# Kernel optimization log

Hardware: AMD Instinct MI355X
Metric: run time of the kernel (lower is better)

## Reference

```python
import jax, jax.numpy as jnp
import numpy as np

VOCAB, EMB, HID = 50257, 256, 512
B, S = 64, 512


def setup_inputs() -> dict:
    key = jax.random.key(0)
    ks = jax.random.split(key, 11)
    sc = 0.05
    return {
        "inputs": jax.random.randint(ks[0], (B, S), 0, VOCAB, dtype=jnp.int32),
        "emb": jax.random.normal(ks[1], (VOCAB, EMB), jnp.float32) * sc,
        "Wi": jax.random.normal(ks[2], (EMB, 4 * HID), jnp.float32) * sc,   # kernel, gate order i|f|g|o (Keras)
        "Wh": jax.random.normal(ks[3], (HID, 4 * HID), jnp.float32) * sc,   # recurrent kernel
        "b": jax.random.normal(ks[4], (4 * HID,), jnp.float32) * sc,
        "W1": jax.random.normal(ks[5], (HID, HID), jnp.float32) * sc,
        "b1": jnp.zeros((HID,), jnp.float32),
        "W2": jax.random.normal(ks[6], (HID, HID), jnp.float32) * sc,
        "b2": jnp.zeros((HID,), jnp.float32),
        "W3": jax.random.normal(ks[7], (HID, VOCAB), jnp.float32) * sc,
        "b3": jnp.zeros((VOCAB,), jnp.float32),
    }


def _lstm_final_h(x, Wi, Wh, b):
    # x: [B, S, E] -> final hidden state [B, H]
    Bsz = x.shape[0]
    H = Wh.shape[0]
    h0 = jnp.zeros((Bsz, H), x.dtype)
    c0 = jnp.zeros((Bsz, H), x.dtype)

    def step(carry, xt):
        h, c = carry
        z = xt @ Wi + h @ Wh + b              # [B, 4H]
        i, f, g, o = jnp.split(z, 4, axis=-1)  # Keras gate order: input, forget, cell, output
        i = jax.nn.sigmoid(i)
        f = jax.nn.sigmoid(f)
        g = jnp.tanh(g)
        o = jax.nn.sigmoid(o)
        c = f * c + i * g
        h = o * jnp.tanh(c)
        return (h, c), None

    (h, _), _ = jax.lax.scan(step, (h0, c0), jnp.swapaxes(x, 0, 1))  # scan over time [S, B, E]
    return h


def reference(inputs, emb, Wi, Wh, b, W1, b1, W2, b2, W3, b3):
    src_emb = emb[inputs]                      # [B, S, E] embedding lookup
    enc_hidden = _lstm_final_h(src_emb, Wi, Wh, b)  # [B, H]
    y = jnp.tanh(enc_hidden @ W1 + b1)
    y = jnp.tanh(y @ W2 + b2)
    logits = y @ W3 + b3                       # [B, vocab]
    return jax.nn.log_softmax(logits, axis=-1)
```

## Files before the change

### kernel.cpp

```cpp
#include <hip/hip_runtime.h>
#include <hip/hip_bf16.h>

#define VOCAB 50257
#define EMBD  256
#define HID   512
#define BATCH 64
#define SEQ   512

typedef short bf16x8 __attribute__((ext_vector_type(8)));
typedef float f32x4  __attribute__((ext_vector_type(4)));

__device__ inline short f2b(float f) {
    union { float f; unsigned u; } v; v.f = f;
    unsigned r = v.u + 0x7FFFu + ((v.u >> 16) & 1u);
    return (short)(r >> 16);
}
__device__ inline unsigned pack2_trunc(float lo, float hi) {
    union { float f; unsigned u; } a, b; a.f = lo; b.f = hi;
    return __builtin_amdgcn_perm(b.u, a.u, 0x07060302);
}
__device__ inline float fast_tanh(float x) {
    x = fminf(fmaxf(x, -15.f), 15.f);
    float e = __expf(2.f * x);
    return (e - 1.f) / (e + 1.f);
}
__device__ inline float fast_sig(float x) { return 1.f / (1.f + __expf(-x)); }

__device__ inline void load_x_frags(const float* __restrict__ emb, int idxv, int quad, bf16x8* Ax) {
#pragma unroll
    for (int kt = 0; kt < 8; ++kt) {
        const float* p = emb + (size_t)idxv * EMBD + kt * 32 + quad * 8;
        float4 e0 = *(const float4*)(p);
        float4 e1 = *(const float4*)(p + 4);
        union { bf16x8 v; unsigned u[4]; } f;
        f.u[0] = pack2_trunc(e0.x, e0.y);
        f.u[1] = pack2_trunc(e0.z, e0.w);
        f.u[2] = pack2_trunc(e1.x, e1.y);
        f.u[3] = pack2_trunc(e1.z, e1.w);
        Ax[kt] = f.v;
    }
}

__global__ __launch_bounds__(256, 1) void lstm_kernel(
    const int* __restrict__ idx, const float* __restrict__ emb,
    const float* __restrict__ Wi, const float* __restrict__ Wh,
    const float* __restrict__ bvec,
    unsigned long long* __restrict__ hbuf ,
    unsigned short* __restrict__ hfinal )
{
    const int wgid = blockIdx.x;
    const int grp  = wgid >> 5;
    const int j    = wgid & 31;
    const int tid  = threadIdx.x;
    const int lane = tid & 63;
    const int gate = tid >> 6;
    const int quad = lane >> 4;
    const int l16  = lane & 15;
    const int col  = gate * HID + j * 16 + l16;
    const int arow = grp * 16 + l16;

    __shared__ float gbuf[4][16][16];
    __shared__ __align__(16) unsigned short hstage[16][HID + 8];

    bf16x8 Bh[16], Bx[8];
#pragma unroll
    for (int kt = 0; kt < 16; ++kt)
#pragma unroll
        for (int i = 0; i < 8; ++i)
            Bh[kt][i] = f2b(Wh[(size_t)(kt * 32 + quad * 8 + i) * 2048 + col]);
#pragma unroll
    for (int kt = 0; kt < 8; ++kt)
#pragma unroll
        for (int i = 0; i < 8; ++i)
            Bx[kt][i] = f2b(Wi[(size_t)(kt * 32 + quad * 8 + i) * 2048 + col]);
    const float bv = bvec[col];

    bf16x8 Ax[8];
    load_x_frags(emb, idx[arow * SEQ], quad, Ax);

    const int srow = gate * 4 + quad;

    const int rr = tid >> 3, u8 = tid & 7, c2 = u8 * 2;
    float cs0 = 0.f, cs1 = 0.f;

    for (int t = 0; t < SEQ; ++t) {
        const unsigned long long* rbase =
            hbuf + ((size_t)((t & 1) * 4 + grp) * 16 + srow) * 256 + l16;

        unsigned long long v[16];
        if (t > 0) {
#pragma unroll
            for (int i = 0; i < 16; ++i)
                v[i] = __hip_atomic_load(rbase + i * 16,
                                         __ATOMIC_RELAXED, __HIP_MEMORY_SCOPE_AGENT);
        }

        f32x4 a0 = {0.f, 0.f, 0.f, 0.f}, a1 = {0.f, 0.f, 0.f, 0.f};
#pragma unroll
        for (int kt = 0; kt < 8; kt += 2) {
            a0 = __builtin_amdgcn_mfma_f32_16x16x32_bf16(Ax[kt],     Bx[kt],     a0, 0, 0, 0);
            a1 = __builtin_amdgcn_mfma_f32_16x16x32_bf16(Ax[kt + 1], Bx[kt + 1], a1, 0, 0, 0);
        }

        if (t > 0) {
            const unsigned tg = (unsigned)t;
            while (true) {
                bool ok = true;
#pragma unroll
                for (int i = 0; i < 16; ++i)
                    ok = ok && ((unsigned)(v[i] >> 32) == tg);
                if (__ballot(ok) == ~0ull) break;
#pragma unroll
                for (int i = 0; i < 16; ++i)
                    v[i] = __hip_atomic_load(rbase + i * 16,
                                             __ATOMIC_RELAXED, __HIP_MEMORY_SCOPE_AGENT);
            }
#pragma unroll
            for (int i = 0; i < 16; ++i)
                *(unsigned*)&hstage[srow][(l16 + i * 16) * 2] = (unsigned)v[i];
        }
        __syncthreads();

        if (t > 0) {
#pragma unroll
            for (int kt = 0; kt < 16; kt += 2) {
                bf16x8 ha = *(const bf16x8*)&hstage[l16][kt * 32 + quad * 8];
                bf16x8 hb = *(const bf16x8*)&hstage[l16][(kt + 1) * 32 + quad * 8];
                a0 = __builtin_amdgcn_mfma_f32_16x16x32_bf16(ha, Bh[kt],     a0, 0, 0, 0);
                a1 = __builtin_amdgcn_mfma_f32_16x16x32_bf16(hb, Bh[kt + 1], a1, 0, 0, 0);
            }
        }

#pragma unroll
        for (int r = 0; r < 4; ++r) {
            float z = a0[r] + a1[r] + bv;
            gbuf[gate][quad * 4 + r][l16] = (gate == 2) ? fast_tanh(z) : fast_sig(z);
        }
        __syncthreads();

        if (tid < 128) {
            float h0, h1;
            {
                float i0 = gbuf[0][rr][c2], f0 = gbuf[1][rr][c2];
                float gg = gbuf[2][rr][c2], o0 = gbuf[3][rr][c2];
                float cc = f0 * cs0 + i0 * gg;
                cs0 = cc;
                h0 = o0 * fast_tanh(cc);
            }
            {
                float i1 = gbuf[0][rr][c2 + 1], f1 = gbuf[1][rr][c2 + 1];
                float gg = gbuf[2][rr][c2 + 1], o1 = gbuf[3][rr][c2 + 1];
                float cc = f1 * cs1 + i1 * gg;
                cs1 = cc;
                h1 = o1 * fast_tanh(cc);
            }
            unsigned pv = (unsigned)(unsigned short)f2b(h0) |
                          ((unsigned)(unsigned short)f2b(h1) << 16);
            unsigned long long val = (unsigned long long)pv |
                                     ((unsigned long long)(unsigned)(t + 1) << 32);
            unsigned long long* dst = hbuf +
                ((size_t)(((t + 1) & 1) * 4 + grp) * 16 + rr) * 256 + j * 8 + u8;
            __hip_atomic_store(dst, val, __ATOMIC_RELAXED, __HIP_MEMORY_SCOPE_AGENT);
            if (t == SEQ - 1)
                *(unsigned*)&hfinal[(size_t)(grp * 16 + rr) * HID + j * 16 + c2] = pv;
        }

        if (t + 1 < SEQ) {
            int nx = idx[arow * SEQ + t + 1];
            load_x_frags(emb, nx, quad, Ax);
        }
    }
}

__global__ __launch_bounds__(256, 1) void gemm_tanh_kernel(
    const unsigned short* __restrict__ A, const float* __restrict__ W,
    const float* __restrict__ bias, unsigned short* __restrict__ out)
{
    const int tid = threadIdx.x, lane = tid & 63, wave = tid >> 6;
    const int quad = lane >> 4, l16 = lane & 15;
    const int col = blockIdx.x * 16 + l16;
    bf16x8 Bw[16];
#pragma unroll
    for (int kt = 0; kt < 16; ++kt)
#pragma unroll
        for (int i = 0; i < 8; ++i)
            Bw[kt][i] = f2b(W[(size_t)(kt * 32 + quad * 8 + i) * HID + col]);
    f32x4 acc = {0.f, 0.f, 0.f, 0.f};
#pragma unroll
    for (int kt = 0; kt < 16; ++kt) {
        bf16x8 a = *(const bf16x8*)(A + (size_t)(wave * 16 + l16) * HID + kt * 32 + quad * 8);
        acc = __builtin_amdgcn_mfma_f32_16x16x32_bf16(a, Bw[kt], acc, 0, 0, 0);
    }
    const float bvv = bias[col];
#pragma unroll
    for (int r = 0; r < 4; ++r) {
        float y = fast_tanh(acc[r] + bvv);
        out[(size_t)(wave * 16 + quad * 4 + r) * HID + col] = (unsigned short)f2b(y);
    }
}

__global__ __launch_bounds__(256, 2) void logits_kernel(
    const unsigned short* __restrict__ A, const float* __restrict__ W3,
    const float* __restrict__ b3, float* __restrict__ outL)
{
    const int tid = threadIdx.x, lane = tid & 63, wave = tid >> 6;
    const int quad = lane >> 4, l16 = lane & 15;
    const int c0 = blockIdx.x * 64;
    const int col = c0 + wave * 16 + l16;
    const bool cok = col < VOCAB;
    const int colc = cok ? col : (VOCAB - 1);

    __shared__ unsigned short wt[256][68];

    f32x4 acc[4];
#pragma unroll
    for (int rt = 0; rt < 4; ++rt) acc[rt] = (f32x4){0.f, 0.f, 0.f, 0.f};

    const int kr = tid >> 4;
    const int cg = (tid & 15) * 4;

    for (int kc = 0; kc < 2; ++kc) {
#pragma unroll 4
        for (int it = 0; it < 16; ++it) {
            const int k = it * 16 + kr;
            const int gc = c0 + cg;
            float4 wv;
            if (gc + 3 < VOCAB) {
                wv = *(const float4*)&W3[(size_t)(kc * 256 + k) * VOCAB + gc];
            } else {
                const float* Wr = &W3[(size_t)(kc * 256 + k) * VOCAB];
                wv.x = (gc + 0 < VOCAB) ? Wr[gc + 0] : 0.f;
                wv.y = (gc + 1 < VOCAB) ? Wr[gc + 1] : 0.f;
                wv.z = (gc + 2 < VOCAB) ? Wr[gc + 2] : 0.f;
                wv.w = (gc + 3 < VOCAB) ? Wr[gc + 3] : 0.f;
            }
            unsigned short* d = &wt[k][cg];
            d[0] = (unsigned short)f2b(wv.x);
            d[1] = (unsigned short)f2b(wv.y);
            d[2] = (unsigned short)f2b(wv.z);
            d[3] = (unsigned short)f2b(wv.w);
        }
        __syncthreads();
        bf16x8 Bw[8];
#pragma unroll
        for (int kt = 0; kt < 8; ++kt)
#pragma unroll
            for (int i = 0; i < 8; ++i)
                Bw[kt][i] = (short)wt[kt * 32 + quad * 8 + i][wave * 16 + l16];
#pragma unroll
        for (int rt = 0; rt < 4; ++rt)
#pragma unroll
            for (int kt = 0; kt < 8; ++kt) {
                bf16x8 a = *(const bf16x8*)(A + (size_t)(rt * 16 + l16) * HID +
                                            kc * 256 + kt * 32 + quad * 8);
                acc[rt] = __builtin_amdgcn_mfma_f32_16x16x32_bf16(a, Bw[kt], acc[rt], 0, 0, 0);
            }
        __syncthreads();
    }
    const float bvv = b3[colc];
    if (cok) {
#pragma unroll
        for (int rt = 0; rt < 4; ++rt)
#pragma unroll
            for (int r = 0; r < 4; ++r)
                outL[(size_t)(rt * 16 + quad * 4 + r) * VOCAB + col] = acc[rt][r] + bvv;
    }
}

__global__ __launch_bounds__(256, 1) void lsm_kernel(
    const float* __restrict__ lg, float* __restrict__ out)
{
    const int row = blockIdx.x;
    const float* L = lg + (size_t)row * VOCAB;
    const float4* L4 = (const float4*)L;
    const int nv4 = VOCAB / 4;

    float m = -1e30f;
    for (int i = threadIdx.x; i < nv4; i += 256) {
        float4 v = L4[i];
        m = fmaxf(fmaxf(fmaxf(m, v.x), fmaxf(v.y, v.z)), v.w);
    }
    if (threadIdx.x == 0) m = fmaxf(m, L[VOCAB - 1]);
#pragma unroll
    for (int o = 32; o; o >>= 1) m = fmaxf(m, __shfl_xor(m, o));
    __shared__ float red[4], red2[4];
    if ((threadIdx.x & 63) == 0) red[threadIdx.x >> 6] = m;
    __syncthreads();
    m = fmaxf(fmaxf(red[0], red[1]), fmaxf(red[2], red[3]));

    float s = 0.f;
    for (int i = threadIdx.x; i < nv4; i += 256) {
        float4 v = L4[i];
        s += __expf(v.x - m) + __expf(v.y - m) + __expf(v.z - m) + __expf(v.w - m);
    }
    if (threadIdx.x == 0) s += __expf(L[VOCAB - 1] - m);
#pragma unroll
    for (int o = 32; o; o >>= 1) s += __shfl_xor(s, o);
    if ((threadIdx.x & 63) == 0) red2[threadIdx.x >> 6] = s;
    __syncthreads();
    s = red2[0] + red2[1] + red2[2] + red2[3];
    const float ls = m + __logf(s);

    float* O = out + (size_t)row * VOCAB;
    float4* O4 = (float4*)O;
    for (int i = threadIdx.x; i < nv4; i += 256) {
        float4 v = L4[i];
        O4[i] = (float4){v.x - ls, v.y - ls, v.z - ls, v.w - ls};
    }
    if (threadIdx.x == 0) O[VOCAB - 1] = L[VOCAB - 1] - ls;
}

extern "C" void kernel_launch(void* const* d_in, const int* in_sizes, int n_in,
                              void* d_out, int out_size, void* d_ws, size_t ws_size,
                              hipStream_t stream) {
    (void)in_sizes; (void)n_in; (void)out_size; (void)ws_size;
    const int*   idx = (const int*)d_in[0];
    const float* emb = (const float*)d_in[1];
    const float* Wi  = (const float*)d_in[2];
    const float* Wh  = (const float*)d_in[3];
    const float* b   = (const float*)d_in[4];
    const float* W1  = (const float*)d_in[5];
    const float* b1  = (const float*)d_in[6];
    const float* W2  = (const float*)d_in[7];
    const float* b2  = (const float*)d_in[8];
    const float* W3  = (const float*)d_in[9];
    const float* b3  = (const float*)d_in[10];
    float* out = (float*)d_out;

    char* w = (char*)d_ws;
    unsigned long long* hbuf   = (unsigned long long*)w;
    unsigned short*     y1     = (unsigned short*)w;
    unsigned short*     y2     = (unsigned short*)(w + 65536);
    unsigned short*     hfinal = (unsigned short*)(w + 262144);
    float*              logits = (float*)(w + 262144);

    lstm_kernel<<<128, 256, 0, stream>>>(idx, emb, Wi, Wh, b, hbuf, hfinal);
    gemm_tanh_kernel<<<HID / 16, 256, 0, stream>>>(hfinal, W1, b1, y1);
    gemm_tanh_kernel<<<HID / 16, 256, 0, stream>>>(y1, W2, b2, y2);
    logits_kernel<<<(VOCAB + 63) / 64, 256, 0, stream>>>(y2, W3, b3, logits);
    lsm_kernel<<<BATCH, 256, 0, stream>>>(logits, out);
}
```

Baseline: 2.183 ms.

## Halve LSTM workgroup count with 8-wave blocks and selective flag polling

The persistent LSTM kernel now runs 64 workgroups of 512 threads, each owning 32 hidden columns instead of 16. This halves the number of cross-workgroup producers each consumer must wait on per timestep. Polling is restructured: each wave reads fewer flagged words, re-polls only words still pending, sleeps briefly between polls, and issues the next step's loads right after publishing its own h. This cuts global polling traffic and synchronisation latency on the serial recurrence, at the cost of more per-block work and higher register pressure from doubling threads per block.

After: 3.550 ms. +62.6%, slower.

```diff
diff --git a/kernel.cpp b/kernel.cpp
--- a/kernel.cpp
+++ b/kernel.cpp
@@ -41,7 +41,7 @@
     }
 }
 
-__global__ __launch_bounds__(256, 1) void lstm_kernel(
+__global__ __launch_bounds__(512, 2) void lstm_kernel(
     const int* __restrict__ idx, const float* __restrict__ emb,
     const float* __restrict__ Wi, const float* __restrict__ Wh,
     const float* __restrict__ bvec,
@@ -49,18 +49,20 @@
     unsigned short* __restrict__ hfinal )
 {
     const int wgid = blockIdx.x;
-    const int grp  = wgid >> 5;
-    const int j    = wgid & 31;
+    const int grp  = wgid >> 4;
+    const int j    = wgid & 15;
     const int tid  = threadIdx.x;
     const int lane = tid & 63;
-    const int gate = tid >> 6;
+    const int wave = tid >> 6;
+    const int gate = wave & 3;
+    const int ch   = wave >> 2;
     const int quad = lane >> 4;
     const int l16  = lane & 15;
-    const int col  = gate * HID + j * 16 + l16;
+    const int col  = gate * HID + j * 32 + ch * 16 + l16;
     const int arow = grp * 16 + l16;
 
-    __shared__ float gbuf[4][16][16];
-    __shared__ __align__(16) unsigned short hstage[16][HID + 8];
+    __shared__ float gbuf[4][16][33];
+    __shared__ __align__(16) unsigned short hstage[16][528];
 
     bf16x8 Bh[16], Bx[8];
 #pragma unroll
@@ -78,22 +80,17 @@
     bf16x8 Ax[8];
     load_x_frags(emb, idx[arow * SEQ], quad, Ax);
 
-    const int srow = gate * 4 + quad;
-
-    const int rr = tid >> 3, u8 = tid & 7, c2 = u8 * 2;
+    const int prow  = wave * 2 + (lane >> 5);
+    const int punit = lane & 31;
+
+    const int rr = tid >> 4, u16 = tid & 15, c2 = u16 * 2;
     float cs0 = 0.f, cs1 = 0.f;
+
+    unsigned long long v[8];
 
     for (int t = 0; t < SEQ; ++t) {
         const unsigned long long* rbase =
-            hbuf + ((size_t)((t & 1) * 4 + grp) * 16 + srow) * 256 + l16;
-
-        unsigned long long v[16];
-        if (t > 0) {
-#pragma unroll
-            for (int i = 0; i < 16; ++i)
-                v[i] = __hip_atomic_load(rbase + i * 16,
-                                         __ATOMIC_RELAXED, __HIP_MEMORY_SCOPE_AGENT);
-        }
+            hbuf + ((size_t)((t & 1) * 4 + grp) * 16 + prow) * 256 + punit;
 
         f32x4 a0 = {0.f, 0.f, 0.f, 0.f}, a1 = {0.f, 0.f, 0.f, 0.f};
 #pragma unroll
@@ -104,20 +101,25 @@
 
         if (t > 0) {
             const unsigned tg = (unsigned)t;
+            unsigned pend = 0xFFu;
             while (true) {
-                bool ok = true;
-#pragma unroll
-                for (int i = 0; i < 16; ++i)
-                    ok = ok && ((unsigned)(v[i] >> 32) == tg);
-                if (__ballot(ok) == ~0ull) break;
-#pragma unroll
-                for (int i = 0; i < 16; ++i)
-                    v[i] = __hip_atomic_load(rbase + i * 16,
-                                             __ATOMIC_RELAXED, __HIP_MEMORY_SCOPE_AGENT);
-            }
-#pragma unroll
-            for (int i = 0; i < 16; ++i)
-                *(unsigned*)&hstage[srow][(l16 + i * 16) * 2] = (unsigned)v[i];
+                unsigned np = 0;
+#pragma unroll
+                for (int i = 0; i < 8; ++i)
+                    if ((pend & (1u << i)) && (unsigned)(v[i] >> 32) != tg)
+                        np |= (1u << i);
+                pend = np;
+                if (__ballot(pend != 0) == 0ull) break;
+                __builtin_amdgcn_s_sleep(1);
+#pragma unroll
+                for (int i = 0; i < 8; ++i)
+                    if (__ballot(pend & (1u << i)) != 0ull)
+                        v[i] = __hip_atomic_load(rbase + i * 32,
+                                                 __ATOMIC_RELAXED, __HIP_MEMORY_SCOPE_AGENT);
+            }
+#pragma unroll
+            for (int i = 0; i < 8; ++i)
+                *(unsigned*)&hstage[prow][(punit + 32 * i) * 2] = (unsigned)v[i];
         }
         __syncthreads();
 
@@ -134,11 +136,11 @@
 #pragma unroll
         for (int r = 0; r < 4; ++r) {
             float z = a0[r] + a1[r] + bv;
-            gbuf[gate][quad * 4 + r][l16] = (gate == 2) ? fast_tanh(z) : fast_sig(z);
+            gbuf[gate][quad * 4 + r][ch * 16 + l16] = (gate == 2) ? fast_tanh(z) : fast_sig(z);
         }
         __syncthreads();
 
-        if (tid < 128) {
+        if (tid < 256) {
             float h0, h1;
             {
                 float i0 = gbuf[0][rr][c2], f0 = gbuf[1][rr][c2];
@@ -159,13 +161,19 @@
             unsigned long long val = (unsigned long long)pv |
                                      ((unsigned long long)(unsigned)(t + 1) << 32);
             unsigned long long* dst = hbuf +
-                ((size_t)(((t + 1) & 1) * 4 + grp) * 16 + rr) * 256 + j * 8 + u8;
+                ((size_t)(((t + 1) & 1) * 4 + grp) * 16 + rr) * 256 + j * 16 + u16;
             __hip_atomic_store(dst, val, __ATOMIC_RELAXED, __HIP_MEMORY_SCOPE_AGENT);
             if (t == SEQ - 1)
-                *(unsigned*)&hfinal[(size_t)(grp * 16 + rr) * HID + j * 16 + c2] = pv;
+                *(unsigned*)&hfinal[(size_t)(grp * 16 + rr) * HID + j * 32 + c2] = pv;
         }
 
         if (t + 1 < SEQ) {
+            const unsigned long long* nb =
+                hbuf + ((size_t)(((t + 1) & 1) * 4 + grp) * 16 + prow) * 256 + punit;
+#pragma unroll
+            for (int i = 0; i < 8; ++i)
+                v[i] = __hip_atomic_load(nb + i * 32,
+                                         __ATOMIC_RELAXED, __HIP_MEMORY_SCOPE_AGENT);
             int nx = idx[arow * SEQ + t + 1];
             load_x_frags(emb, nx, quad, Ax);
         }
@@ -334,7 +342,7 @@
     unsigned short*     hfinal = (unsigned short*)(w + 262144);
     float*              logits = (float*)(w + 262144);
 
-    lstm_kernel<<<128, 256, 0, stream>>>(idx, emb, Wi, Wh, b, hbuf, hfinal);
+    lstm_kernel<<<64, 512, 0, stream>>>(idx, emb, Wi, Wh, b, hbuf, hfinal);
     gemm_tanh_kernel<<<HID / 16, 256, 0, stream>>>(hfinal, W1, b1, y1);
     gemm_tanh_kernel<<<HID / 16, 256, 0, stream>>>(y1, W2, b2, y2);
     logits_kernel<<<(VOCAB + 63) / 64, 256, 0, stream>>>(y2, W3, b3, logits);
```
